# Kernel tuning notes

Measured on AMD Instinct MI355X. Metric: run time of the kernel, lower is better.

## Reference

```python
import jax, jax.numpy as jnp
import numpy as np

IN_DIM = 3
GRID_LEVEL = 7
FEAT_DIMS = 2
HIDDEN = 128
BOUND = 1.0
W0_SINE = 56.0  # n_levels**feature_dims - n_levels = 8**2 - 8
N = 131072


def setup_inputs() -> dict:
    key = jax.random.key(0)
    ks = jax.random.split(key, 10)
    return {
        "in_pos": jax.random.uniform(ks[0], (N, IN_DIM), jnp.float32, -1.0, 1.0),
        "grid_feats": jax.random.uniform(ks[1], (N, IN_DIM + GRID_LEVEL * FEAT_DIMS), jnp.float32),
        "ffn_A": jax.random.normal(ks[2], (GRID_LEVEL, FEAT_DIMS, HIDDEN), jnp.float32) * 5.0,
        "ffn_sigma": jnp.ones((GRID_LEVEL,), jnp.float32),
        "W0": jax.random.uniform(ks[3], (HIDDEN, IN_DIM), jnp.float32, -1.0 / IN_DIM, 1.0 / IN_DIM),
        "b0": jax.random.uniform(ks[4], (HIDDEN,), jnp.float32, -1.0 / IN_DIM, 1.0 / IN_DIM),
        "W_mid": jax.random.uniform(ks[5], (GRID_LEVEL, HIDDEN, HIDDEN), jnp.float32) * (2.0 * np.sqrt(6.0 / HIDDEN) / W0_SINE) - np.sqrt(6.0 / HIDDEN) / W0_SINE,
        "b_mid": jnp.zeros((GRID_LEVEL, HIDDEN), jnp.float32),
        "W_high": jax.random.uniform(ks[6], (GRID_LEVEL, HIDDEN, HIDDEN), jnp.float32) * (2.0 * np.sqrt(6.0 / HIDDEN) / W0_SINE) - np.sqrt(6.0 / HIDDEN) / W0_SINE,
        "b_high": jnp.zeros((GRID_LEVEL, HIDDEN), jnp.float32),
    }


def reference(in_pos, grid_feats, ffn_A, ffn_sigma, W0, b0, W_mid, b_mid, W_high, b_high):
    x = in_pos / BOUND                     # [N, 3], in [-1, 1]
    pos01 = (in_pos + BOUND) / (2.0 * BOUND)  # [N, 3], in [0, 1]

    # grid branch: slice off the first in_dim columns, reshape to [L, N, F]
    gx = grid_feats[..., IN_DIM:].reshape(-1, GRID_LEVEL, FEAT_DIMS).transpose(1, 0, 2)
    A = ffn_A * ffn_sigma[:, None, None]   # [L, F, H]
    grid_x = jnp.sin(jnp.einsum('lnf,lfh->lnh', gx, (2.0 * jnp.pi) * A))  # [L, N, H]

    # first SIREN layer
    x = jnp.sin(W0_SINE * (x @ W0.T + b0))  # [N, H]

    def step(carry, layer):
        x, buf = carry
        Wm, bm, Wh, bh, g = layer
        x = jnp.sin(W0_SINE * (x @ Wm.T + bm))
        x = g + x                                  # residual add of grid features
        buf = buf + jnp.sin(W0_SINE * (x @ Wh.T + bh))  # high-freq accumulation
        return (x, buf), None

    buf0 = jnp.zeros((x.shape[0], HIDDEN), x.dtype)
    (_, buf), _ = jax.lax.scan(step, (x, buf0), (W_mid, b_mid, W_high, b_high, grid_x))

    return jnp.concatenate([pos01, buf / GRID_LEVEL], axis=-1)  # [N, 3 + 128]
```

## Files before the change

### kernel.cpp

```cpp
#include <hip/hip_runtime.h>
#include <hip/hip_bf16.h>


typedef __bf16 bf16_t;
typedef __attribute__((ext_vector_type(8))) __bf16 bf16x8;
typedef __attribute__((ext_vector_type(4))) float f32x4;
typedef __attribute__((ext_vector_type(16))) float f32x16;

#define C56R 8.9126768f
#define INV7 0.14285714285714285f

#define OFF_WMF   0
#define OFF_WMFLO 229376
#define OFF_WHF   458752
#define OFF_EPM   688128

union ChunkU { bf16x8 v; unsigned int d[4]; };

__device__ __forceinline__ unsigned short bfbits(float x) {
  bf16_t b = (bf16_t)x;
  return __builtin_bit_cast(unsigned short, b);
}
__device__ __forceinline__ float bf2f(unsigned short u) {
  return __builtin_bit_cast(float, (unsigned int)u << 16);
}
__device__ __forceinline__ void pack2(float v0, float v1,
                                      unsigned int& ph, unsigned int& pl) {
  unsigned short h0 = bfbits(v0), h1 = bfbits(v1);
  ph = (unsigned int)h0 | ((unsigned int)h1 << 16);
  float l0 = v0 - bf2f(h0), l1 = v1 - bf2f(h1);
  pl = (unsigned int)bfbits(l0) | ((unsigned int)bfbits(l1) << 16);
}

__global__ void ffb_prep(const float* __restrict__ ffnA, const float* __restrict__ sigma,
                         const float* __restrict__ Wm, const float* __restrict__ bm,
                         const float* __restrict__ Wh, const float* __restrict__ bh,
                         unsigned char* __restrict__ ws) {
  int i = blockIdx.x * 256 + threadIdx.x;
  bf16_t* wmf = (bf16_t*)(ws + OFF_WMF);
  bf16_t* wml = (bf16_t*)(ws + OFF_WMFLO);
  bf16_t* whf = (bf16_t*)(ws + OFF_WHF);
  {
    int j    = i & 7;
    int lane = (i >> 3) & 63;
    int kc   = (i >> 9) & 7;
    int mt   = (i >> 12) & 3;
    int it   = i >> 14;
    int ho   = (mt << 5) + (lane & 31);
    int hin  = (kc << 4) + ((lane >> 5) << 3) + j;
    int src  = (it << 14) + (ho << 7) + hin;
    float w  = Wm[src];
    bf16_t h = (bf16_t)w;
    wmf[i] = h;
    wml[i] = (bf16_t)(w - (float)h);
    whf[i] = (bf16_t)Wh[src];
  }
  if (i < 896) {
    int r  = i & 15;
    int mt = (i >> 4) & 3;
    int hf = (i >> 6) & 1;
    int it = i >> 7;
    int h  = (mt << 5) + (r & 3) + ((r >> 2) << 3) + (hf << 2);
    float sg = sigma[it];
    f32x4 e;
    e.x = ffnA[it * 256 + h] * sg;
    e.y = ffnA[it * 256 + 128 + h] * sg;
    e.z = C56R * bm[it * 128 + h];
    e.w = C56R * bh[it * 128 + h];
    ((f32x4*)(ws + OFF_EPM))[i] = e;
  }
}

__launch_bounds__(256, 3)
__global__ void ffb_main(const float* __restrict__ pos,
                         const float* __restrict__ gfeat,
                         const float* __restrict__ W0,
                         const float* __restrict__ b0,
                         const unsigned char* __restrict__ ws,
                         float* __restrict__ out) {
  __shared__ __align__(16) unsigned char smem[30720];
  unsigned char* sX = smem;
  f32x4* sEPv = (f32x4*)(smem + 16384);
  float* sEPf = (float*)(smem + 16384);

  const int tid  = threadIdx.x;
  const int L    = tid & 63;
  const int sub  = tid >> 6;
  const int p    = L & 31;
  const int hf   = L >> 5;
  const int n    = (blockIdx.x << 5) + p;

  const bf16_t* __restrict__ WMH = (const bf16_t*)(ws + OFF_WMF);
  const bf16_t* __restrict__ WML = (const bf16_t*)(ws + OFF_WMFLO);
  const bf16_t* __restrict__ WHF = (const bf16_t*)(ws + OFF_WHF);
  const f32x4*  __restrict__ EPM = (const f32x4*)(ws + OFF_EPM);

  bf16x8 mh[8], ml[8], hfr[8];
  {
    const bf16_t* wh0 = WMH + (sub << 12) + (L << 3);
    const bf16_t* wl0 = WML + (sub << 12) + (L << 3);
    #pragma unroll
    for (int kc = 0; kc < 8; ++kc) {
      mh[kc] = *(const bf16x8*)(wh0 + (kc << 9));
      ml[kc] = *(const bf16x8*)(wl0 + (kc << 9));
    }
  }

  #pragma unroll
  for (int c = 0; c < 4; ++c) {
    int idx = tid + (c << 8);
    if (idx < 896) sEPv[idx] = EPM[idx];
  }

  const float p0 = pos[n * 3 + 0], p1 = pos[n * 3 + 1], p2 = pos[n * 3 + 2];
  if (sub == 0 && hf == 0) {
    out[(size_t)n * 131 + 0] = (p0 + 1.f) * 0.5f;
    out[(size_t)n * 131 + 1] = (p1 + 1.f) * 0.5f;
    out[(size_t)n * 131 + 2] = (p2 + 1.f) * 0.5f;
  }

  #pragma unroll
  for (int cc = 0; cc < 2; ++cc) {
    const int c = (sub << 1) + cc;
    ChunkU chi, clo;
    #pragma unroll
    for (int jp = 0; jp < 4; ++jp) {
      int h0 = (c << 4) + (hf << 3) + 2 * jp;
      float d0 = __builtin_fmaf(p2, W0[h0*3+2], __builtin_fmaf(p1, W0[h0*3+1], p0 * W0[h0*3+0]));
      float d1 = __builtin_fmaf(p2, W0[h0*3+5], __builtin_fmaf(p1, W0[h0*3+4], p0 * W0[h0*3+3]));
      float v0 = __builtin_amdgcn_sinf(C56R * (d0 + b0[h0]));
      float v1 = __builtin_amdgcn_sinf(C56R * (d1 + b0[h0 + 1]));
      pack2(v0, v1, chi.d[jp], clo.d[jp]);
    }
    *(bf16x8*)(sX + (c << 10) + (L << 4))        = chi.v;
    *(bf16x8*)(sX + 8192 + (c << 10) + (L << 4)) = clo.v;
  }
  __syncthreads();

  f32x16 buf;
  #pragma unroll
  for (int r = 0; r < 16; ++r) buf[r] = 0.f;

  #pragma unroll 1
  for (int it = 0; it < 8; ++it) {
    if (it > 0) {
      f32x16 acc;
      #pragma unroll
      for (int r = 0; r < 16; ++r) acc[r] = 0.f;
      #pragma unroll
      for (int kc = 0; kc < 8; ++kc) {
        bf16x8 xhc = *(const bf16x8*)(sX + (kc << 10) + (L << 4));
        acc = __builtin_amdgcn_mfma_f32_32x32x16_bf16(hfr[kc], xhc, acc, 0, 0, 0);
      }
      const int eb = ((((it - 1) << 1) + hf) << 2) + sub;
      #pragma unroll
      for (int r = 0; r < 16; ++r) {
        float cbh = sEPf[(eb * 16 + r) * 4 + 3];
        buf[r] += __builtin_amdgcn_sinf(__builtin_fmaf(acc[r], C56R, cbh));
      }
    }

    if (it < 7) {
      {
        const bf16_t* wb = WHF + (it << 14) + (sub << 12) + (L << 3);
        #pragma unroll
        for (int kc = 0; kc < 8; ++kc)
          hfr[kc] = *(const bf16x8*)(wb + (kc << 9));
      }

      f32x16 acc;
      #pragma unroll
      for (int r = 0; r < 16; ++r) acc[r] = 0.f;
      #pragma unroll
      for (int kc = 0; kc < 8; ++kc) {
        bf16x8 xhc = *(const bf16x8*)(sX + (kc << 10) + (L << 4));
        bf16x8 xlc = *(const bf16x8*)(sX + 8192 + (kc << 10) + (L << 4));
        acc = __builtin_amdgcn_mfma_f32_32x32x16_bf16(mh[kc], xhc, acc, 0, 0, 0);
        acc = __builtin_amdgcn_mfma_f32_32x32x16_bf16(ml[kc], xhc, acc, 0, 0, 0);
        acc = __builtin_amdgcn_mfma_f32_32x32x16_bf16(mh[kc], xlc, acc, 0, 0, 0);
      }

      if (it < 6) {
        const bf16_t* wh = WMH + ((it + 1) << 14) + (sub << 12) + (L << 3);
        const bf16_t* wl = WML + ((it + 1) << 14) + (sub << 12) + (L << 3);
        #pragma unroll
        for (int kc = 0; kc < 8; ++kc) {
          mh[kc] = *(const bf16x8*)(wh + (kc << 9));
          ml[kc] = *(const bf16x8*)(wl + (kc << 9));
        }
      }

      __syncthreads();

      const float g0 = gfeat[n * 17 + 3 + 2 * it];
      const float g1 = gfeat[n * 17 + 4 + 2 * it];
      const int eb = (((it << 1) + hf) << 2) + sub;
      #pragma unroll
      for (int rp = 0; rp < 8; ++rp) {
        const int r = 2 * rp;
        f32x4 e0 = sEPv[eb * 16 + r];
        f32x4 e1 = sEPv[eb * 16 + r + 1];
        float sg0 = __builtin_amdgcn_sinf(__builtin_amdgcn_fractf(__builtin_fmaf(g1, e0.y, g0 * e0.x)));
        float sg1 = __builtin_amdgcn_sinf(__builtin_amdgcn_fractf(__builtin_fmaf(g1, e1.y, g0 * e1.x)));
        float sm0 = __builtin_amdgcn_sinf(__builtin_fmaf(acc[r],     C56R, e0.z));
        float sm1 = __builtin_amdgcn_sinf(__builtin_fmaf(acc[r + 1], C56R, e1.z));
        unsigned int phv, plv;
        pack2(sg0 + sm0, sg1 + sm1, phv, plv);
        const int h   = (sub << 5) + (r & 3) + ((r >> 2) << 3) + (hf << 2);
        const int off = ((h >> 4) << 10) + ((p + (((h >> 3) & 1) << 5)) << 4) + ((h & 7) << 1);
        *(unsigned int*)(sX + off)        = phv;
        *(unsigned int*)(sX + 8192 + off) = plv;
      }
      __syncthreads();
    }
  }

  float* op = out + (size_t)n * 131 + 3;
  #pragma unroll
  for (int r = 0; r < 16; ++r) {
    const int h = (sub << 5) + (r & 3) + ((r >> 2) << 3) + (hf << 2);
    op[h] = buf[r] * INV7;
  }
}

extern "C" void kernel_launch(void* const* d_in, const int* in_sizes, int n_in,
                              void* d_out, int out_size, void* d_ws, size_t ws_size,
                              hipStream_t stream) {
  (void)in_sizes; (void)n_in; (void)out_size; (void)ws_size;
  const float* pos   = (const float*)d_in[0];
  const float* gfeat = (const float*)d_in[1];
  const float* ffnA  = (const float*)d_in[2];
  const float* sigma = (const float*)d_in[3];
  const float* W0    = (const float*)d_in[4];
  const float* b0    = (const float*)d_in[5];
  const float* Wm    = (const float*)d_in[6];
  const float* bm    = (const float*)d_in[7];
  const float* Wh    = (const float*)d_in[8];
  const float* bh    = (const float*)d_in[9];
  float* out = (float*)d_out;
  unsigned char* ws = (unsigned char*)d_ws;

  hipLaunchKernelGGL(ffb_prep, dim3(448), dim3(256), 0, stream,
                     ffnA, sigma, Wm, bm, Wh, bh, ws);
  hipLaunchKernelGGL(ffb_main, dim3(4096), dim3(256), 0, stream,
                     pos, gfeat, W0, b0, ws, out);
}
```

Baseline: 266.2 us.

## Pad LDS epilogue table, widen LDS stores, use lightweight barriers and full unroll

Replaces __syncthreads with a waitcnt plus s_barrier helper and inserts sched_barriers to pin the global weight prefetches relative to the MFMA loops. The epilogue-parameter table in LDS is padded to a 17-entry stride to reduce bank conflicts. The activation write-back now packs four outputs into 64-bit LDS stores instead of 32-bit ones. The iteration loop is fully unrolled, which removes loop overhead but may raise register pressure or code size against the 3-blocks-per-CU launch bound.

After: 534.0 us. 101% more time.

```diff
diff --git a/kernel.cpp b/kernel.cpp
--- a/kernel.cpp
+++ b/kernel.cpp
@@ -30,6 +30,10 @@
   ph = (unsigned int)h0 | ((unsigned int)h1 << 16);
   float l0 = v0 - bf2f(h0), l1 = v1 - bf2f(h1);
   pl = (unsigned int)bfbits(l0) | ((unsigned int)bfbits(l1) << 16);
+}
+__device__ __forceinline__ void lds_barrier() {
+  asm volatile("s_waitcnt lgkmcnt(0)" ::: "memory");
+  __builtin_amdgcn_s_barrier();
 }
 
 __global__ void ffb_prep(const float* __restrict__ ffnA, const float* __restrict__ sigma,
@@ -78,7 +82,7 @@
                          const float* __restrict__ b0,
                          const unsigned char* __restrict__ ws,
                          float* __restrict__ out) {
-  __shared__ __align__(16) unsigned char smem[30720];
+  __shared__ __align__(16) unsigned char smem[31616];
   unsigned char* sX = smem;
   f32x4* sEPv = (f32x4*)(smem + 16384);
   float* sEPf = (float*)(smem + 16384);
@@ -105,11 +109,12 @@
       ml[kc] = *(const bf16x8*)(wl0 + (kc << 9));
     }
   }
+  __builtin_amdgcn_sched_barrier(0);
 
   #pragma unroll
   for (int c = 0; c < 4; ++c) {
     int idx = tid + (c << 8);
-    if (idx < 896) sEPv[idx] = EPM[idx];
+    if (idx < 896) sEPv[(idx >> 4) * 17 + (idx & 15)] = EPM[idx];
   }
 
   const float p0 = pos[n * 3 + 0], p1 = pos[n * 3 + 1], p2 = pos[n * 3 + 2];
@@ -135,13 +140,13 @@
     *(bf16x8*)(sX + (c << 10) + (L << 4))        = chi.v;
     *(bf16x8*)(sX + 8192 + (c << 10) + (L << 4)) = clo.v;
   }
-  __syncthreads();
+  lds_barrier();
 
   f32x16 buf;
   #pragma unroll
   for (int r = 0; r < 16; ++r) buf[r] = 0.f;
 
-  #pragma unroll 1
+  #pragma unroll
   for (int it = 0; it < 8; ++it) {
     if (it > 0) {
       f32x16 acc;
@@ -152,10 +157,10 @@
         bf16x8 xhc = *(const bf16x8*)(sX + (kc << 10) + (L << 4));
         acc = __builtin_amdgcn_mfma_f32_32x32x16_bf16(hfr[kc], xhc, acc, 0, 0, 0);
       }
-      const int eb = ((((it - 1) << 1) + hf) << 2) + sub;
+      const int eb17 = ((((it - 1) << 1) + hf) * 4 + sub) * 17;
       #pragma unroll
       for (int r = 0; r < 16; ++r) {
-        float cbh = sEPf[(eb * 16 + r) * 4 + 3];
+        float cbh = sEPf[(eb17 + r) * 4 + 3];
         buf[r] += __builtin_amdgcn_sinf(__builtin_fmaf(acc[r], C56R, cbh));
       }
     }
@@ -167,6 +172,7 @@
         for (int kc = 0; kc < 8; ++kc)
           hfr[kc] = *(const bf16x8*)(wb + (kc << 9));
       }
+      __builtin_amdgcn_sched_barrier(0);
 
       f32x16 acc;
       #pragma unroll
@@ -189,29 +195,37 @@
           ml[kc] = *(const bf16x8*)(wl + (kc << 9));
         }
       }
-
-      __syncthreads();
+      __builtin_amdgcn_sched_barrier(0);
+
+      lds_barrier();
 
       const float g0 = gfeat[n * 17 + 3 + 2 * it];
       const float g1 = gfeat[n * 17 + 4 + 2 * it];
-      const int eb = (((it << 1) + hf) << 2) + sub;
-      #pragma unroll
-      for (int rp = 0; rp < 8; ++rp) {
-        const int r = 2 * rp;
-        f32x4 e0 = sEPv[eb * 16 + r];
-        f32x4 e1 = sEPv[eb * 16 + r + 1];
-        float sg0 = __builtin_amdgcn_sinf(__builtin_amdgcn_fractf(__builtin_fmaf(g1, e0.y, g0 * e0.x)));
-        float sg1 = __builtin_amdgcn_sinf(__builtin_amdgcn_fractf(__builtin_fmaf(g1, e1.y, g0 * e1.x)));
-        float sm0 = __builtin_amdgcn_sinf(__builtin_fmaf(acc[r],     C56R, e0.z));
-        float sm1 = __builtin_amdgcn_sinf(__builtin_fmaf(acc[r + 1], C56R, e1.z));
-        unsigned int phv, plv;
-        pack2(sg0 + sm0, sg1 + sm1, phv, plv);
-        const int h   = (sub << 5) + (r & 3) + ((r >> 2) << 3) + (hf << 2);
-        const int off = ((h >> 4) << 10) + ((p + (((h >> 3) & 1) << 5)) << 4) + ((h & 7) << 1);
-        *(unsigned int*)(sX + off)        = phv;
-        *(unsigned int*)(sX + 8192 + off) = plv;
-      }
-      __syncthreads();
+      const int eb17 = (((it << 1) + hf) * 4 + sub) * 17;
+      #pragma unroll
+      for (int q = 0; q < 4; ++q) {
+        const int r0 = q << 2;
+        float v[4];
+        #pragma unroll
+        for (int k = 0; k < 4; ++k) {
+          const int r = r0 + k;
+          f32x4 e = sEPv[eb17 + r];
+          float sg = __builtin_amdgcn_sinf(__builtin_amdgcn_fractf(__builtin_fmaf(g1, e.y, g0 * e.x)));
+          float sm = __builtin_amdgcn_sinf(__builtin_fmaf(acc[r], C56R, e.z));
+          v[k] = sg + sm;
+        }
+        unsigned int ph0, pl0, ph1, pl1;
+        pack2(v[0], v[1], ph0, pl0);
+        pack2(v[2], v[3], ph1, pl1);
+        unsigned long long qh = (unsigned long long)ph0 | ((unsigned long long)ph1 << 32);
+        unsigned long long ql = (unsigned long long)pl0 | ((unsigned long long)pl1 << 32);
+        const int c   = (sub << 1) + (r0 >> 3);
+        const int bit = (r0 >> 2) & 1;
+        const int off = (c << 10) + ((p + (bit << 5)) << 4) + (hf << 3);
+        *(unsigned long long*)(sX + off)        = qh;
+        *(unsigned long long*)(sX + 8192 + off) = ql;
+      }
+      lds_barrier();
     }
   }
 
```
